# Kernel optimization log

Hardware: AMD Instinct MI355X
Metric: run time of the kernel (lower is better)

## Reference

```python
import jax, jax.numpy as jnp
import numpy as np

E = 2048   # embed_dim
H = 16     # num_heads
D = E // H # head_dim = 128
ROPE_BASE = 10000.0


def setup_inputs() -> dict:
    key = jax.random.key(0)
    ks = jax.random.split(key, 9)
    s = 0.02
    x = jax.random.normal(ks[0], (2, 2048, E), dtype=jnp.float32)
    Wq = jax.random.normal(ks[1], (E, E), dtype=jnp.float32) * s
    bq = jax.random.normal(ks[2], (E,), dtype=jnp.float32) * s
    Wk = jax.random.normal(ks[3], (E, E), dtype=jnp.float32) * s
    bk = jax.random.normal(ks[4], (E,), dtype=jnp.float32) * s
    Wv = jax.random.normal(ks[5], (E, E), dtype=jnp.float32) * s
    bv = jax.random.normal(ks[6], (E,), dtype=jnp.float32) * s
    Wo = jax.random.normal(ks[7], (E, E), dtype=jnp.float32) * s
    bo = jax.random.normal(ks[8], (E,), dtype=jnp.float32) * s
    return {"x": x, "Wq": Wq, "bq": bq, "Wk": Wk, "bk": bk,
            "Wv": Wv, "bv": bv, "Wo": Wo, "bo": bo}


def _rope_cos_sin(seq_len, dtype):
    inv_freq = 1.0 / (ROPE_BASE ** (jnp.arange(0, D, 2, dtype=jnp.float32) / D))
    pos = jnp.arange(seq_len, dtype=jnp.float32)
    freqs = pos[:, None] * inv_freq[None, :]          # (S, D/2)
    emb = jnp.concatenate([freqs, freqs], axis=-1)    # (S, D)
    return jnp.cos(emb).astype(dtype), jnp.sin(emb).astype(dtype)


def _rotate_half(t):
    t1, t2 = jnp.split(t, 2, axis=-1)
    return jnp.concatenate([-t2, t1], axis=-1)


def reference(x, Wq, bq, Wk, bk, Wv, bv, Wo, bo):
    B, S, _ = x.shape
    # QKV projections (torch Linear: x @ W.T + b)
    q = (x @ Wq.T + bq).reshape(B, S, H, D).transpose(0, 2, 1, 3)  # (B,H,S,D)
    k = (x @ Wk.T + bk).reshape(B, S, H, D).transpose(0, 2, 1, 3)
    v = (x @ Wv.T + bv).reshape(B, S, H, D).transpose(0, 2, 1, 3)
    # RoPE
    cos, sin = _rope_cos_sin(S, x.dtype)              # (S, D) each
    q = q * cos + _rotate_half(q) * sin
    k = k * cos + _rotate_half(k) * sin
    # Causal scaled dot-product attention
    scale = 1.0 / jnp.sqrt(jnp.asarray(D, dtype=x.dtype))
    scores = jnp.einsum('bhqd,bhkd->bhqk', q, k) * scale
    causal = jnp.tril(jnp.ones((S, S), dtype=bool))
    scores = jnp.where(causal, scores, jnp.asarray(-jnp.inf, dtype=x.dtype))
    attn = jax.nn.softmax(scores, axis=-1)
    out = jnp.einsum('bhqk,bhkd->bhqd', attn, v)      # (B,H,S,D)
    out = out.transpose(0, 2, 1, 3).reshape(B, S, E)
    return out @ Wo.T + bo
```

## Files before the change

### kernel.cpp

```cpp
#include <hip/hip_runtime.h>
#include <math.h>

typedef __bf16 bf16;
typedef __attribute__((ext_vector_type(2))) __bf16 bf16x2;
typedef __attribute__((ext_vector_type(4))) __bf16 bf16x4;
typedef __attribute__((ext_vector_type(8))) __bf16 bf16x8;
typedef __attribute__((ext_vector_type(4))) float f32x4;

#define GLD16(g, l) __builtin_amdgcn_global_load_lds( \
    (const __attribute__((address_space(1))) void*)(g), \
    (__attribute__((address_space(3))) void*)(l), 16, 0, 0)

template<int N> __device__ __forceinline__ void wait_vm() {
  static_assert(N == 0 || N == 4 || N == 6, "");
  if constexpr (N == 0) asm volatile("s_waitcnt vmcnt(0)" ::: "memory");
  else if constexpr (N == 4) asm volatile("s_waitcnt vmcnt(4)" ::: "memory");
  else asm volatile("s_waitcnt vmcnt(6)" ::: "memory");
}

__global__ void prep_kernel(const float* __restrict__ x,
                            const float* __restrict__ Wq, const float* __restrict__ Wk,
                            const float* __restrict__ Wv, const float* __restrict__ Wo,
                            const float* __restrict__ bq, const float* __restrict__ bk,
                            const float* __restrict__ bv,
                            bf16* __restrict__ xb, bf16* __restrict__ wqkv, bf16* __restrict__ wob,
                            float* __restrict__ biasq, float* __restrict__ cost, float* __restrict__ sint) {
  const int bid = blockIdx.x, t = threadIdx.x;
  if (bid < 24576) {
    const float* src;
    bf16* dst;
    int i;
    if (bid < 8192)       { src = x;  dst = xb;                    i = bid * 256 + t; }
    else if (bid < 12288) { src = Wq; dst = wqkv;                  i = (bid - 8192) * 256 + t; }
    else if (bid < 16384) { src = Wk; dst = wqkv + 2048 * 2048;    i = (bid - 12288) * 256 + t; }
    else if (bid < 20480) { src = Wv; dst = wqkv + 2 * 2048 * 2048; i = (bid - 16384) * 256 + t; }
    else                  { src = Wo; dst = wob;                   i = (bid - 20480) * 256 + t; }
    float4 f = ((const float4*)src)[i];
    bf16x4 o;
    o[0] = (bf16)f.x; o[1] = (bf16)f.y; o[2] = (bf16)f.z; o[3] = (bf16)f.w;
    ((bf16x4*)dst)[i] = o;
  } else if (bid < 25088) {
    int i = (bid - 24576) * 256 + t;
    int s = i >> 6, d = i & 63;
    float inv = powf(10000.0f, -(float)d / 64.0f);
    float ang = (float)s * inv;
    cost[i] = cosf(ang);
    sint[i] = sinf(ang);
  } else {
    int i = (bid - 25088) * 256 + t;
    biasq[i] = (i < 2048) ? bq[i] : (i < 4096 ? bk[i - 2048] : bv[i - 4096]);
  }
}

__global__ void rope_tv_kernel(const bf16* __restrict__ qkv,
                               const float* __restrict__ cost, const float* __restrict__ sint,
                               bf16* __restrict__ kr, bf16* __restrict__ vt) {
  __shared__ bf16 Vl[64 * 72];
  const int t = threadIdx.x;
  if (blockIdx.x < 4096) {
    int idx = blockIdx.x * 256 + t;
    int dp = idx & 15;
    int h = (idx >> 4) & 15;
    int s = (idx >> 8) & 2047;
    int b = idx >> 19;
    int d0 = dp * 4;
    const bf16* row = qkv + ((size_t)(b * 2048 + s) * 6144) + 2048 + h * 128;
    bf16x4 klo = *(const bf16x4*)&row[d0];
    bf16x4 khi = *(const bf16x4*)&row[d0 + 64];
    float4 c4 = *(const float4*)&cost[(s << 6) + d0];
    float4 s4 = *(const float4*)&sint[(s << 6) + d0];
    float cf[4] = {c4.x, c4.y, c4.z, c4.w};
    float sf[4] = {s4.x, s4.y, s4.z, s4.w};
    bf16x4 olo, ohi;
#pragma unroll
    for (int j = 0; j < 4; ++j) {
      float kl = (float)klo[j], kh = (float)khi[j];
      olo[j] = (bf16)(kl * cf[j] - kh * sf[j]);
      ohi[j] = (bf16)(kh * cf[j] + kl * sf[j]);
    }
    bf16* orow = kr + (((size_t)(b * 16 + h) * 2048 + s) * 128);
    *(bf16x4*)&orow[d0] = olo;
    *(bf16x4*)&orow[d0 + 64] = ohi;
  } else {
    int vbid = blockIdx.x - 4096;
    const int dt = vbid & 1, st = (vbid >> 1) & 31, bh = vbid >> 6;
    const int b = bh >> 4, h = bh & 15;
    const bf16* src = qkv + ((size_t)(b * 2048 + st * 64) * 6144) + 4096 + h * 128 + dt * 64;
    bf16* dst = vt + ((size_t)bh * 128 + dt * 64) * 2048 + st * 64;
#pragma unroll
    for (int i = 0; i < 2; ++i) {
      int c = i * 256 + t;
      int r = c >> 3, c0 = (c & 7) * 8;
      *(bf16x8*)&Vl[r * 72 + c0] = *(const bf16x8*)&src[(size_t)r * 6144 + c0];
    }
    __syncthreads();
#pragma unroll
    for (int i = 0; i < 2; ++i) {
      int c = i * 256 + t;
      int r = c >> 3, c0 = (c & 7) * 8;
      bf16x8 v;
#pragma unroll
      for (int j = 0; j < 8; ++j) v[j] = Vl[(c0 + j) * 72 + r];
      *(bf16x8*)&dst[(size_t)r * 2048 + c0] = v;
    }
  }
}

template<int BN, bool OUT_BF16>
__global__ __launch_bounds__(256, 2)
void gemm4w_kernel(const bf16* __restrict__ A, const bf16* __restrict__ B,
                   const float* __restrict__ bias, void* __restrict__ Cp,
                   int M, int N, int K) {
  constexpr int NB = BN / 64;
  constexpr int NR = BN / 32;
  __shared__ bf16 Al[2][128 * 64];
  __shared__ bf16 Bl[2][NB][64 * 64];
  const int t = threadIdx.x;
  const int wid = t >> 6, lane = t & 63;
  const int wr = wid >> 1, wc = wid & 1;
  const int lr = lane & 15, lk = lane >> 4;
  const int flat = (int)blockIdx.x;
  const int xcd = flat & 7, r0 = flat >> 3;
  const int tm = xcd * 4 + (r0 & 3);
  const int tn = r0 >> 2;
  const bf16* Ab = A + (size_t)tm * 128 * K;
  const bf16* Bb = B + (size_t)tn * BN * K;
  const int NT = K >> 6;

  auto stageA = [&](int bp, int h, int kt) {
#pragma unroll
    for (int q = 0; q < 2; ++q) {
      int e = q * 256 + t;
      int r = e >> 3, c = e & 7;
      GLD16(Ab + (size_t)(h * 64 + r) * K + kt * 64 + ((c ^ (r & 7)) << 3),
            &Al[bp][h * 4096 + e * 8]);
    }
  };
  auto stageB = [&](int bp, int unit, int kt) {
#pragma unroll
    for (int q = 0; q < 2; ++q) {
      int e = q * 256 + t;
      int r = e >> 3, c = e & 7;
      GLD16(Bb + (size_t)(unit * 64 + r) * K + kt * 64 + ((c ^ (r & 7)) << 3),
            &Bl[bp][unit][e * 8]);
    }
  };

  f32x4 acc[4][NR] = {};

#pragma unroll
  for (int un = 0; un < NB; ++un) stageB(0, un, 0);
  stageA(0, 0, 0); stageA(0, 1, 0);
  if (NT > 1) {
#pragma unroll
    for (int un = 0; un < NB; ++un) stageB(1, un, 1);
    wait_vm<2 * NB>();
  } else {
    wait_vm<0>();
  }
  __builtin_amdgcn_s_barrier();
  __builtin_amdgcn_sched_barrier(0);

  for (int u = 0; u < NT; ++u) {
    const int p = u & 1;
    bf16x8 bfr[NR][2];
#pragma unroll
    for (int j = 0; j < 4; ++j) {
      if (j == 0) {
#pragma unroll
        for (int n = 0; n < NR; ++n)
#pragma unroll
          for (int kk = 0; kk < 2; ++kk) {
            int rb = wc * (NR * 16) + n * 16 + lr;
            bfr[n][kk] = *(const bf16x8*)&Bl[p][rb >> 6][(rb & 63) * 64 + ((((kk << 2) | lk) ^ (rb & 7)) << 3)];
          }
      }
      bf16x8 afr[2];
      {
        int row = wr * 64 + j * 16 + lr;
#pragma unroll
        for (int kk = 0; kk < 2; ++kk)
          afr[kk] = *(const bf16x8*)&Al[p][row * 64 + ((((kk << 2) | lk) ^ (row & 7)) << 3)];
      }
      if (j == 0)      { if (u + 1 < NT) stageA(p ^ 1, 0, u + 1); }
      else if (j == 1) { if (u + 1 < NT) stageA(p ^ 1, 1, u + 1); }
      else if (j == 2) {
        if (u + 2 < NT) {
#pragma unroll
          for (int un = 0; un < NB - 1; ++un) stageB(p, un, u + 2);
        }
      } else {
        if (u + 2 < NT) stageB(p, NB - 1, u + 2);
      }
      __builtin_amdgcn_s_barrier();
      asm volatile("s_waitcnt lgkmcnt(0)" ::: "memory");
      __builtin_amdgcn_sched_barrier(0);
      __builtin_amdgcn_s_setprio(1);
#pragma unroll
      for (int n = 0; n < NR; ++n)
#pragma unroll
        for (int kk = 0; kk < 2; ++kk)
          acc[j][n] = __builtin_amdgcn_mfma_f32_16x16x32_bf16(afr[kk], bfr[n][kk], acc[j][n], 0, 0, 0);
      __builtin_amdgcn_s_setprio(0);
      __builtin_amdgcn_sched_barrier(0);
      if (j == 3) {
        if (u + 2 < NT) { wait_vm<2 * NB>(); }
        else            { wait_vm<0>(); }
      }
      __builtin_amdgcn_s_barrier();
      __builtin_amdgcn_sched_barrier(0);
    }
  }

  const int rbase = tm * 128 + wr * 64, cbase = tn * BN + wc * (NR * 16);
#pragma unroll
  for (int n = 0; n < NR; ++n) {
    int col = cbase + n * 16 + lr;
    float bvl = bias[col];
#pragma unroll
    for (int m = 0; m < 4; ++m) {
#pragma unroll
      for (int rr = 0; rr < 4; ++rr) {
        int row = rbase + m * 16 + lk * 4 + rr;
        float v = acc[m][n][rr] + bvl;
        if (OUT_BF16) ((bf16*)Cp)[(size_t)row * N + col] = (bf16)v;
        else          ((float*)Cp)[(size_t)row * N + col] = v;
      }
    }
  }
}

__global__ __launch_bounds__(256, 3)
void attn_kernel(const bf16* __restrict__ qkv, const bf16* __restrict__ Kc,
                 const bf16* __restrict__ Vtg, const float* __restrict__ cost,
                 const float* __restrict__ sint, bf16* __restrict__ O, int S) {
  __shared__ bf16 Kl[2][64 * 128];
  __shared__ bf16 Vt[2][128 * 64];
  __shared__ bf16 Pl[4][16 * 64];
  const int t = threadIdx.x, wid = t >> 6, lane = t & 63;
  const int lr = lane & 15, lk = lane >> 4;
  const int flat = (int)blockIdx.x;
  const int xcd = flat & 7, kk2 = flat >> 3;
  const int bh = xcd * 4 + (kk2 >> 4);
  const int b = bh >> 4, h = bh & 15;
  const int NQ = S >> 6;
  const int qtA = kk2 & 15, qtB = NQ - 1 - qtA;
  const int ntA = qtA + 1, ntB = qtB + 1, total = ntA + ntB;
  const bf16* Kb = Kc + (size_t)bh * S * 128;
  const bf16* Vb = Vtg + (size_t)bh * 128 * S;
  const float scale = 0.08838834764831845f;

  bf16x8 qf[4];
  auto loadQ = [&](int q0) {
    int qrow = q0 + wid * 16 + lr;
    const bf16* qp = qkv + (size_t)(b * 2048 + qrow) * 6144 + h * 128;
    bf16x8 raw[4];
#pragma unroll
    for (int kb = 0; kb < 4; ++kb) raw[kb] = *(const bf16x8*)&qp[kb * 32 + lk * 8];
#pragma unroll
    for (int kb = 0; kb < 4; ++kb) {
      const float* cb = cost + (qrow << 6) + ((kb & 1) << 5) + lk * 8;
      const float* sb = sint + (qrow << 6) + ((kb & 1) << 5) + lk * 8;
#pragma unroll
      for (int j = 0; j < 8; ++j) {
        float qv = (float)raw[kb][j];
        float qo = (float)raw[kb ^ 2][j];
        float rot = (kb < 2) ? -qo : qo;
        qf[kb][j] = (bf16)(qv * cb[j] + rot * sb[j]);
      }
    }
  };
  auto stage = [&](int buf, int kv0) {
#pragma unroll
    for (int c = 0; c < 4; ++c) {
      int fc = c * 256 + t;
      int kvr = fc >> 4, cc = fc & 15;
      GLD16(Kb + (size_t)(kv0 + kvr) * 128 + (cc ^ (kvr & 7)) * 8, &Kl[buf][fc * 8]);
      int dr = fc >> 3, c2 = fc & 7;
      GLD16(Vb + (size_t)dr * S + kv0 + (c2 ^ (dr & 7)) * 8, &Vt[buf][fc * 8]);
    }
  };

  f32x4 o[8] = {};
  float mrun[4], lrun[4];
#pragma unroll
  for (int r = 0; r < 4; ++r) { mrun[r] = -INFINITY; lrun[r] = 0.f; }

  loadQ(qtA * 64);
  stage(0, 0);
  __syncthreads();
  int cur = 0;
  for (int ti = 0; ti < total; ++ti) {
    if (ti + 1 < total) {
      int tn = ti + 1;
      stage(cur ^ 1, ((tn < ntA) ? tn : tn - ntA) * 64);
    }
    __builtin_amdgcn_sched_barrier(0);
    const bool isA = ti < ntA;
    const int tt = isA ? ti : ti - ntA;
    const int nt = isA ? ntA : ntB;
    const int q0 = (isA ? qtA : qtB) * 64;
    const int kv0 = tt * 64;
    f32x4 sa[4];
    __builtin_amdgcn_s_setprio(1);
#pragma unroll
    for (int n = 0; n < 4; ++n) {
      sa[n] = (f32x4){0.f, 0.f, 0.f, 0.f};
      int kvl = n * 16 + lr;
#pragma unroll
      for (int kb = 0; kb < 4; ++kb) {
        bf16x8 kf = *(const bf16x8*)&Kl[cur][kvl * 128 + (((kb << 2) | lk) ^ (kvl & 7)) * 8];
        sa[n] = __builtin_amdgcn_mfma_f32_16x16x32_bf16(qf[kb], kf, sa[n], 0, 0, 0);
      }
    }
    __builtin_amdgcn_s_setprio(0);
    float p[4][4];
    float tmax[4] = {-INFINITY, -INFINITY, -INFINITY, -INFINITY};
    const bool lastTile = (tt == nt - 1);
#pragma unroll
    for (int n = 0; n < 4; ++n)
#pragma unroll
      for (int r = 0; r < 4; ++r) {
        float s = sa[n][r] * scale;
        if (lastTile) {
          int kvg = kv0 + n * 16 + lr;
          int qg = q0 + wid * 16 + lk * 4 + r;
          if (kvg > qg) s = -INFINITY;
        }
        p[n][r] = s;
        tmax[r] = fmaxf(tmax[r], s);
      }
#pragma unroll
    for (int r = 0; r < 4; ++r)
#pragma unroll
      for (int off = 1; off < 16; off <<= 1)
        tmax[r] = fmaxf(tmax[r], __shfl_xor(tmax[r], off));
    float alpha[4], rsum[4];
#pragma unroll
    for (int r = 0; r < 4; ++r) {
      float mnew = fmaxf(mrun[r], tmax[r]);
      alpha[r] = __expf(mrun[r] - mnew);
      mrun[r] = mnew;
      rsum[r] = 0.f;
#pragma unroll
      for (int n = 0; n < 4; ++n) {
        p[n][r] = __expf(p[n][r] - mnew);
        rsum[r] += p[n][r];
      }
    }
#pragma unroll
    for (int r = 0; r < 4; ++r) {
#pragma unroll
      for (int off = 1; off < 16; off <<= 1)
        rsum[r] += __shfl_xor(rsum[r], off);
      lrun[r] = lrun[r] * alpha[r] + rsum[r];
    }
#pragma unroll
    for (int n8 = 0; n8 < 8; ++n8)
#pragma unroll
      for (int r = 0; r < 4; ++r)
        o[n8][r] *= alpha[r];
#pragma unroll
    for (int n = 0; n < 4; ++n)
#pragma unroll
      for (int r = 0; r < 4; ++r) {
        int row = lk * 4 + r, col = n * 16 + lr;
        Pl[wid][(row * 64 + col) ^ ((row & 7) << 3)] = (bf16)p[n][r];
      }
    __builtin_amdgcn_s_setprio(1);
#pragma unroll
    for (int kb2 = 0; kb2 < 2; ++kb2) {
      bf16x8 pf = *(const bf16x8*)&Pl[wid][(lr * 64 + kb2 * 32 + lk * 8) ^ ((lr & 7) << 3)];
#pragma unroll
      for (int n8 = 0; n8 < 8; ++n8) {
        int dcol = n8 * 16 + lr;
        bf16x8 vf = *(const bf16x8*)&Vt[cur][(dcol * 64 + kb2 * 32 + lk * 8) ^ ((dcol & 7) << 3)];
        o[n8] = __builtin_amdgcn_mfma_f32_16x16x32_bf16(pf, vf, o[n8], 0, 0, 0);
      }
    }
    __builtin_amdgcn_s_setprio(0);
    if (ti == ntA - 1) {
#pragma unroll
      for (int r = 0; r < 4; ++r) {
        float rl = 1.0f / lrun[r];
        int row = qtA * 64 + wid * 16 + lk * 4 + r;
        size_t base = ((size_t)(b * S + row)) * 2048 + h * 128;
#pragma unroll
        for (int n8 = 0; n8 < 8; ++n8)
          O[base + n8 * 16 + lr] = (bf16)(o[n8][r] * rl);
      }
#pragma unroll
      for (int n8 = 0; n8 < 8; ++n8) o[n8] = (f32x4){0.f, 0.f, 0.f, 0.f};
#pragma unroll
      for (int r = 0; r < 4; ++r) { mrun[r] = -INFINITY; lrun[r] = 0.f; }
      loadQ(qtB * 64);
    }
    __syncthreads();
    cur ^= 1;
  }
#pragma unroll
  for (int r = 0; r < 4; ++r) {
    float rl = 1.0f / lrun[r];
    int row = qtB * 64 + wid * 16 + lk * 4 + r;
    size_t base = ((size_t)(b * S + row)) * 2048 + h * 128;
#pragma unroll
    for (int n8 = 0; n8 < 8; ++n8)
      O[base + n8 * 16 + lr] = (bf16)(o[n8][r] * rl);
  }
}


extern "C" void kernel_launch(void* const* d_in, const int* in_sizes, int n_in,
                              void* d_out, int out_size, void* d_ws, size_t ws_size,
                              hipStream_t stream) {
  const float* x  = (const float*)d_in[0];
  const float* Wq = (const float*)d_in[1];
  const float* bq = (const float*)d_in[2];
  const float* Wk = (const float*)d_in[3];
  const float* bk = (const float*)d_in[4];
  const float* Wv = (const float*)d_in[5];
  const float* bv = (const float*)d_in[6];
  const float* Wo = (const float*)d_in[7];
  const float* bo = (const float*)d_in[8];

  char* ws = (char*)d_ws;
  bf16* xb     = (bf16*)(ws);
  bf16* wqkv   = (bf16*)(ws + 16777216);
  bf16* wob    = (bf16*)(ws + 41943040);
  bf16* qkv    = (bf16*)(ws + 50331648);
  bf16* kr     = (bf16*)(ws + 100663296);
  bf16* vt     = (bf16*)(ws + 117440512);
  float* biasq = (float*)(ws + 134217728);
  float* cost  = (float*)(ws + 134242304);
  float* sint  = (float*)(ws + 134766592);
  bf16* attn_out = xb;

  prep_kernel<<<25112, 256, 0, stream>>>(x, Wq, Wk, Wv, Wo, bq, bk, bv,
                                         xb, wqkv, wob, biasq, cost, sint);
  gemm4w_kernel<192, true><<<1024, 256, 0, stream>>>(xb, wqkv, biasq, qkv, 4096, 6144, 2048);
  rope_tv_kernel<<<6144, 256, 0, stream>>>(qkv, cost, sint, kr, vt);
  attn_kernel<<<512, 256, 0, stream>>>(qkv, kr, vt, cost, sint, attn_out, 2048);
  gemm4w_kernel<128, false><<<512, 256, 0, stream>>>(attn_out, wob, bo, (float*)d_out, 4096, 2048, 2048);
}
```

Measured before the change: 287.4 us.

## Split GEMM k-tile into two k-halves phases with fewer barriers

Reorganizes the projection GEMM main loop so each k-tile runs as two phases, one per 32-wide k half, covering all four M sub-tiles. This replaces the previous four phases, one per M sub-tile. That cuts the number of workgroup barriers and lgkmcnt waits per k-tile and issues longer uninterrupted MFMA runs. The A and B global-to-LDS staging is regrouped into the two phases. The cost is more A fragments held in registers at once, and slightly less fine-grained interleaving of loads with compute.

```diff
diff --git a/kernel.cpp b/kernel.cpp
--- a/kernel.cpp
+++ b/kernel.cpp
@@ -145,6 +145,14 @@
             &Bl[bp][unit][e * 8]);
     }
   };
+  auto readA = [&](int bp, int m, int kk) -> bf16x8 {
+    int row = wr * 64 + m * 16 + lr;
+    return *(const bf16x8*)&Al[bp][row * 64 + ((((kk << 2) | lk) ^ (row & 7)) << 3)];
+  };
+  auto readB = [&](int bp, int n, int kk) -> bf16x8 {
+    int rb = wc * (NR * 16) + n * 16 + lr;
+    return *(const bf16x8*)&Bl[bp][rb >> 6][(rb & 63) * 64 + ((((kk << 2) | lk) ^ (rb & 7)) << 3)];
+  };
 
   f32x4 acc[4][NR] = {};
 
@@ -163,53 +171,46 @@
 
   for (int u = 0; u < NT; ++u) {
     const int p = u & 1;
-    bf16x8 bfr[NR][2];
-#pragma unroll
-    for (int j = 0; j < 4; ++j) {
-      if (j == 0) {
-#pragma unroll
-        for (int n = 0; n < NR; ++n)
-#pragma unroll
-          for (int kk = 0; kk < 2; ++kk) {
-            int rb = wc * (NR * 16) + n * 16 + lr;
-            bfr[n][kk] = *(const bf16x8*)&Bl[p][rb >> 6][(rb & 63) * 64 + ((((kk << 2) | lk) ^ (rb & 7)) << 3)];
-          }
-      }
-      bf16x8 afr[2];
-      {
-        int row = wr * 64 + j * 16 + lr;
-#pragma unroll
-        for (int kk = 0; kk < 2; ++kk)
-          afr[kk] = *(const bf16x8*)&Al[p][row * 64 + ((((kk << 2) | lk) ^ (row & 7)) << 3)];
-      }
-      if (j == 0)      { if (u + 1 < NT) stageA(p ^ 1, 0, u + 1); }
-      else if (j == 1) { if (u + 1 < NT) stageA(p ^ 1, 1, u + 1); }
-      else if (j == 2) {
-        if (u + 2 < NT) {
-#pragma unroll
-          for (int un = 0; un < NB - 1; ++un) stageB(p, un, u + 2);
-        }
-      } else {
-        if (u + 2 < NT) stageB(p, NB - 1, u + 2);
-      }
-      __builtin_amdgcn_s_barrier();
-      asm volatile("s_waitcnt lgkmcnt(0)" ::: "memory");
-      __builtin_amdgcn_sched_barrier(0);
-      __builtin_amdgcn_s_setprio(1);
+    bf16x8 bfr[NR][2], afr[4];
+#pragma unroll
+    for (int n = 0; n < NR; ++n)
+#pragma unroll
+      for (int kk = 0; kk < 2; ++kk) bfr[n][kk] = readB(p, n, kk);
+#pragma unroll
+    for (int m = 0; m < 4; ++m) afr[m] = readA(p, m, 0);
+    if (u + 1 < NT) { stageA(p ^ 1, 0, u + 1); stageA(p ^ 1, 1, u + 1); }
+    __builtin_amdgcn_s_barrier();
+    asm volatile("s_waitcnt lgkmcnt(0)" ::: "memory");
+    __builtin_amdgcn_sched_barrier(0);
+    __builtin_amdgcn_s_setprio(1);
+#pragma unroll
+    for (int m = 0; m < 4; ++m)
 #pragma unroll
       for (int n = 0; n < NR; ++n)
-#pragma unroll
-        for (int kk = 0; kk < 2; ++kk)
-          acc[j][n] = __builtin_amdgcn_mfma_f32_16x16x32_bf16(afr[kk], bfr[n][kk], acc[j][n], 0, 0, 0);
-      __builtin_amdgcn_s_setprio(0);
-      __builtin_amdgcn_sched_barrier(0);
-      if (j == 3) {
-        if (u + 2 < NT) { wait_vm<2 * NB>(); }
-        else            { wait_vm<0>(); }
-      }
-      __builtin_amdgcn_s_barrier();
-      __builtin_amdgcn_sched_barrier(0);
-    }
+        acc[m][n] = __builtin_amdgcn_mfma_f32_16x16x32_bf16(afr[m], bfr[n][0], acc[m][n], 0, 0, 0);
+    __builtin_amdgcn_s_setprio(0);
+    __builtin_amdgcn_sched_barrier(0);
+#pragma unroll
+    for (int m = 0; m < 4; ++m) afr[m] = readA(p, m, 1);
+    if (u + 2 < NT) {
+#pragma unroll
+      for (int un = 0; un < NB; ++un) stageB(p, un, u + 2);
+    }
+    __builtin_amdgcn_s_barrier();
+    asm volatile("s_waitcnt lgkmcnt(0)" ::: "memory");
+    __builtin_amdgcn_sched_barrier(0);
+    __builtin_amdgcn_s_setprio(1);
+#pragma unroll
+    for (int m = 0; m < 4; ++m)
+#pragma unroll
+      for (int n = 0; n < NR; ++n)
+        acc[m][n] = __builtin_amdgcn_mfma_f32_16x16x32_bf16(afr[m], bfr[n][1], acc[m][n], 0, 0, 0);
+    __builtin_amdgcn_s_setprio(0);
+    __builtin_amdgcn_sched_barrier(0);
+    if (u + 2 < NT) { wait_vm<2 * NB>(); }
+    else            { wait_vm<0>(); }
+    __builtin_amdgcn_s_barrier();
+    __builtin_amdgcn_sched_barrier(0);
   }
 
   const int rbase = tm * 128 + wr * 64, cbase = tn * BN + wc * (NR * 16);
```

Measured after the change: 274.7 us. -4.4%, faster.
